# Kernel tuning notes

Hardware: AMD Instinct MI355X
Metric: run time of the kernel (lower is better)

The kernel has to match this reference:

```python
import math
import jax, jax.numpy as jnp
import numpy as np

DIM = 1024
B, T = 4, 2048


def setup_inputs() -> dict:
    key = jax.random.key(0)
    ks = jax.random.split(key, 7)
    std = 0.02
    x = jax.random.normal(ks[0], (B, T, DIM), dtype=jnp.float32)
    Wq = jax.random.normal(ks[1], (DIM, DIM), dtype=jnp.float32) * std
    Wk = jax.random.normal(ks[2], (DIM, DIM), dtype=jnp.float32) * std
    Wv = jax.random.normal(ks[3], (DIM, DIM), dtype=jnp.float32) * std
    Wo = jax.random.normal(ks[4], (DIM, DIM), dtype=jnp.float32) * std
    # decay_proj: torch init is zero weight, bias = decay_init; use a small random
    # weight so the data-dependent decay path is exercised.
    Wd = jax.random.normal(ks[5], (1, DIM), dtype=jnp.float32) * std
    bd = jnp.full((1,), 3.0, dtype=jnp.float32)  # decay_init
    out_scale = jnp.full((1,), 0.1, dtype=jnp.float32)
    return {"x": x, "Wq": Wq, "Wk": Wk, "Wv": Wv, "Wo": Wo,
            "Wd": Wd, "bd": bd, "out_scale": out_scale}


def reference(x, Wq, Wk, Wv, Wo, Wd, bd, out_scale):
    Bsz, Tlen, dim = x.shape
    scale = 1.0 / math.sqrt(dim)
    # torch Linear: y = x @ W.T
    q = jnp.einsum('btd,ed->bte', x, Wq)
    k = jnp.einsum('btd,ed->bte', x, Wk)
    v = jnp.einsum('btd,ed->bte', x, Wv)
    scores = jnp.einsum('btd,bsd->bts', q, k) * scale            # [B,T,T]
    decay_logits = jnp.einsum('btd,ed->bte', x, Wd)[..., 0] + bd  # [B,T]
    decay = jax.nn.sigmoid(decay_logits)
    pos = jnp.arange(Tlen)
    diff = pos[None, :] - pos[:, None]                            # diff[i,j] = j - i
    causal = (diff > 0).astype(x.dtype)                           # [T,T]
    log_decay = jnp.log(decay + 1e-8)                             # [B,T]
    dist = jnp.clip(diff.astype(x.dtype) - 1.0, 0.0)              # [T,T]
    # log_weights[b,i,j] = log_decay[b,j] * dist[i,j]
    log_weights = log_decay[:, None, :] * dist[None, :, :]
    weights = jnp.exp(log_weights) * causal[None, :, :]
    scores = scores * weights
    retrieved = jnp.einsum('bts,bsd->btd', scores, v)
    out = jnp.einsum('btd,ed->bte', retrieved, Wo) * out_scale
    return out
```

## Files before the change

### kernel.cpp

```cpp
#include <hip/hip_runtime.h>


using u16 = unsigned short;
typedef __bf16 bf16x8 __attribute__((ext_vector_type(8)));
typedef float f32x4 __attribute__((ext_vector_type(4)));

__device__ inline u16 f2bf(float f) {
  unsigned u = __builtin_bit_cast(unsigned, f);
  unsigned r = (u + 0x7FFFu + ((u >> 16) & 1u)) >> 16;
  return (u16)r;
}

__device__ inline void gload16(const u16* g, u16* l) {
  __builtin_amdgcn_global_load_lds(
      (const __attribute__((address_space(1))) void*)g,
      (__attribute__((address_space(3))) void*)l, 16, 0, 0);
}

__global__ __launch_bounds__(256) void xcast_decay(const float* __restrict__ x,
    u16* __restrict__ Xbf, const float* __restrict__ Wd,
    const float* __restrict__ bd, float* __restrict__ ldec) {
  int row = blockIdx.x;
  int t = threadIdx.x;
  float4 f = reinterpret_cast<const float4*>(x + (size_t)row * 1024)[t];
  float4 g = reinterpret_cast<const float4*>(Wd)[t];
  ushort4 o;
  o.x = f2bf(f.x); o.y = f2bf(f.y); o.z = f2bf(f.z); o.w = f2bf(f.w);
  reinterpret_cast<ushort4*>(Xbf + (size_t)row * 1024)[t] = o;
  float s = f.x * g.x + f.y * g.y + f.z * g.z + f.w * g.w;
  #pragma unroll
  for (int off = 32; off > 0; off >>= 1) s += __shfl_xor(s, off);
  __shared__ float red[4];
  if ((t & 63) == 0) red[t >> 6] = s;
  __syncthreads();
  if (t == 0) {
    float tot = red[0] + red[1] + red[2] + red[3];
    float dec = 1.f / (1.f + expf(-(tot + bd[0])));
    ldec[row] = logf(dec + 1e-8f);
  }
}

__global__ __launch_bounds__(256) void wcast(const float* __restrict__ Wq,
    const float* __restrict__ Wk, const float* __restrict__ Wv,
    const float* __restrict__ Wo, u16* __restrict__ Wall) {
  int b = blockIdx.x;
  int m = b >> 10;
  const float* src = (m == 0) ? Wq : (m == 1) ? Wk : (m == 2) ? Wv : Wo;
  int i = ((b & 1023) * 256 + threadIdx.x) * 4;
  float4 f = *reinterpret_cast<const float4*>(src + i);
  ushort4 o;
  o.x = f2bf(f.x); o.y = f2bf(f.y); o.z = f2bf(f.z); o.w = f2bf(f.w);
  *reinterpret_cast<ushort4*>(Wall + (size_t)m * 1048576 + i) = o;
}

template <int EPI>
__global__ __launch_bounds__(512, 2)
void gemm3(const u16* __restrict__ Ab, const u16* __restrict__ Bb,
           void* __restrict__ Cv, int lda, int ldb, int ldc, int K,
           int tiles_n, int diag, const float* __restrict__ ldec,
           const float* __restrict__ scale_ptr,
           long long abs_, long long bbs_, long long cbs_, int ld_stride) {
  __shared__ __align__(16) u16 lds2[73728];

  const int batch = blockIdx.y;
  const u16* A = Ab + (size_t)batch * abs_;
  const u16* B = Bb + (size_t)batch * bbs_;

  const int it = blockIdx.x / tiles_n;
  const int jt = blockIdx.x % tiles_n;
  if (EPI == 1 && jt < 2 * it) return;
  const int m0 = it * 256, n0 = jt * 128;

  const int tid = threadIdx.x;
  const int lane = tid & 63;
  const int w = tid >> 6;
  const int wm = w >> 1, wn = w & 1;
  const int l15 = lane & 15, lhi = lane >> 4;
  const int lr8 = lane >> 3;
  const int schunk = (lane & 7) ^ lr8;

  const int kt0 = diag ? it * 4 : 0;
  const int nkt = K / 64;
  const int span = nkt - kt0;

  f32x4 acc[4][4];
  #pragma unroll
  for (int i = 0; i < 4; ++i)
    #pragma unroll
    for (int j = 0; j < 4; ++j) acc[i][j] = (f32x4)0.f;

  auto stage = [&](int kt, int buf) {
    const size_t kb = (size_t)kt * 64 + schunk * 8;
    u16* lb = &lds2[buf * 24576];
    #pragma unroll
    for (int u = 0; u < 4; ++u)
      gload16(A + (size_t)(m0 + u * 64 + w * 8 + lr8) * lda + kb,
              lb + (u * 64 + w * 8) * 64);
    #pragma unroll
    for (int u = 0; u < 2; ++u)
      gload16(B + (size_t)(n0 + u * 64 + w * 8 + lr8) * ldb + kb,
              lb + 16384 + (u * 64 + w * 8) * 64);
  };

  stage(kt0, 0);
  stage(kt0 + 1, 1);
  asm volatile("s_waitcnt vmcnt(6)" ::: "memory");
  __builtin_amdgcn_s_barrier();

  int bR = 0, bS = 2;
  for (int t = 0; t < span; ++t) {
    const u16* baseA = &lds2[bR * 24576];
    const u16* baseB = baseA + 16384;

    bf16x8 af[4][2], bv[4][2];
    #pragma unroll
    for (int mi = 0; mi < 4; ++mi) {
      int r = wm * 64 + mi * 16 + l15;
      #pragma unroll
      for (int kk = 0; kk < 2; ++kk) {
        int s = (kk * 4 + lhi) ^ (r & 7);
        af[mi][kk] = *reinterpret_cast<const bf16x8*>(&baseA[r * 64 + s * 8]);
      }
    }
    #pragma unroll
    for (int ni = 0; ni < 4; ++ni) {
      int r = wn * 64 + ni * 16 + l15;
      #pragma unroll
      for (int kk = 0; kk < 2; ++kk) {
        int s = (kk * 4 + lhi) ^ (r & 7);
        bv[ni][kk] = *reinterpret_cast<const bf16x8*>(&baseB[r * 64 + s * 8]);
      }
    }

    int t2 = t + 2; if (t2 >= span) t2 = span - 1;
    stage(kt0 + t2, bS);

    __builtin_amdgcn_s_setprio(1);
    #pragma unroll
    for (int kk = 0; kk < 2; ++kk)
      #pragma unroll
      for (int mi = 0; mi < 4; ++mi)
        #pragma unroll
        for (int ni = 0; ni < 4; ++ni)
          acc[mi][ni] = __builtin_amdgcn_mfma_f32_16x16x32_bf16(
              af[mi][kk], bv[ni][kk], acc[mi][ni], 0, 0, 0);
    __builtin_amdgcn_s_setprio(0);

    asm volatile("s_waitcnt vmcnt(6)" ::: "memory");
    __builtin_amdgcn_s_barrier();

    bR = (bR == 2) ? 0 : bR + 1;
    bS = (bS == 2) ? 0 : bS + 1;
  }
  asm volatile("s_waitcnt vmcnt(0)" ::: "memory");

  if (EPI == 0) {
    u16* C = (u16*)Cv + (size_t)batch * cbs_;
    #pragma unroll
    for (int mi = 0; mi < 4; ++mi)
      #pragma unroll
      for (int q = 0; q < 4; ++q) {
        int row = m0 + wm * 64 + mi * 16 + lhi * 4 + q;
        u16* crow = C + (size_t)row * ldc + n0 + wn * 64 + l15;
        #pragma unroll
        for (int ni = 0; ni < 4; ++ni) crow[ni * 16] = f2bf(acc[mi][ni][q]);
      }
  } else if (EPI == 1) {
    u16* C = (u16*)Cv + (size_t)batch * cbs_;
    const float* ldp = ldec + (size_t)batch * ld_stride;
    float ldv[4];
    #pragma unroll
    for (int ni = 0; ni < 4; ++ni) ldv[ni] = ldp[n0 + wn * 64 + ni * 16 + l15];
    const float sc = 0.03125f;
    #pragma unroll
    for (int mi = 0; mi < 4; ++mi)
      #pragma unroll
      for (int q = 0; q < 4; ++q) {
        int row = m0 + wm * 64 + mi * 16 + lhi * 4 + q;
        u16* crow = C + (size_t)row * ldc + n0 + wn * 64 + l15;
        #pragma unroll
        for (int ni = 0; ni < 4; ++ni) {
          int col = n0 + wn * 64 + ni * 16 + l15;
          int d = col - row;
          float wgt = (d > 0) ? expf(ldv[ni] * (float)(d - 1)) : 0.f;
          crow[ni * 16] = f2bf(acc[mi][ni][q] * sc * wgt);
        }
      }
  } else {
    float* C = (float*)Cv + (size_t)batch * cbs_;
    const float sc = scale_ptr[0];
    #pragma unroll
    for (int mi = 0; mi < 4; ++mi)
      #pragma unroll
      for (int q = 0; q < 4; ++q) {
        int row = m0 + wm * 64 + mi * 16 + lhi * 4 + q;
        float* crow = C + (size_t)row * ldc + n0 + wn * 64 + l15;
        #pragma unroll
        for (int ni = 0; ni < 4; ++ni) crow[ni * 16] = acc[mi][ni][q] * sc;
      }
  }
}

extern "C" void kernel_launch(void* const* d_in, const int* in_sizes, int n_in,
                              void* d_out, int out_size, void* d_ws, size_t ws_size,
                              hipStream_t stream) {
  const float* x   = (const float*)d_in[0];
  const float* Wq  = (const float*)d_in[1];
  const float* Wk  = (const float*)d_in[2];
  const float* Wv  = (const float*)d_in[3];
  const float* Wo  = (const float*)d_in[4];
  const float* Wd  = (const float*)d_in[5];
  const float* bd  = (const float*)d_in[6];
  const float* osc = (const float*)d_in[7];
  float* out = (float*)d_out;

  char* ws = (char*)d_ws;
  size_t off = 0;
  u16* Xbf  = (u16*)(ws + off); off += (size_t)8192 * 1024 * 2;
  u16* Wall = (u16*)(ws + off); off += (size_t)4096 * 1024 * 2;
  u16* VT   = (u16*)(ws + off); off += (size_t)1024 * 8192 * 2;
  u16* S    = (u16*)(ws + off); off += (size_t)4 * 2048 * 2048 * 2;
  float* ldec = (float*)(ws + off); off += (size_t)8192 * 4;
  u16* QK   = (u16*)(ws + off); off += (size_t)8192 * 2048 * 2;
  u16* R    = QK;

  u16* Wqk = Wall;
  u16* Wvb = Wall + 2 * 1048576;
  u16* Wob = Wall + 3 * 1048576;

  xcast_decay<<<8192, 256, 0, stream>>>(x, Xbf, Wd, bd, ldec);
  wcast<<<4096, 256, 0, stream>>>(Wq, Wk, Wv, Wo, Wall);

  gemm3<0><<<dim3(32 * 16, 1), 512, 0, stream>>>(
      Xbf, Wqk, QK, 1024, 1024, 2048, 1024, 16, 0, nullptr, nullptr, 0, 0, 0, 0);

  gemm3<0><<<dim3(4 * 64, 1), 512, 0, stream>>>(
      Wvb, Xbf, VT, 1024, 1024, 8192, 1024, 64, 0, nullptr, nullptr, 0, 0, 0, 0);

  gemm3<1><<<dim3(8 * 16, 4), 512, 0, stream>>>(
      QK, QK + 1024, S, 2048, 2048, 2048, 1024, 16, 0, ldec, nullptr,
      4194304LL, 4194304LL, 4194304LL, 2048);

  gemm3<0><<<dim3(8 * 8, 4), 512, 0, stream>>>(
      S, VT, R, 2048, 8192, 1024, 2048, 8, 1, nullptr, nullptr,
      4194304LL, 2048LL, 2097152LL, 0);

  gemm3<2><<<dim3(32 * 8, 1), 512, 0, stream>>>(
      R, Wob, out, 1024, 1024, 1024, 1024, 8, 0, nullptr, osc, 0, 0, 0, 0);
}
```

Measured before the change: 177.3 us.

## Split GEMM into wide and 128x128 causal kernels with compact triangular grids

Splits the single GEMM template into two kernels. gemmW keeps 256x128 tiles for the projection GEMMs and interleaves half-tile loads with each k-substep. gemmN uses 128x128 tiles for the causal score and score×V GEMMs. The score GEMM now enumerates only upper-triangular tiles instead of launching and early-exiting lower ones, and the score×V GEMM reverses row order on half the batches to balance triangular work. This cuts wasted blocks and improves load balance, but drops the occupancy hint to one block per CU and adds extra barriers.

```diff
diff --git a/kernel.cpp b/kernel.cpp
--- a/kernel.cpp
+++ b/kernel.cpp
@@ -54,12 +54,11 @@
 }
 
 template <int EPI>
-__global__ __launch_bounds__(512, 2)
-void gemm3(const u16* __restrict__ Ab, const u16* __restrict__ Bb,
+__global__ __launch_bounds__(512, 1)
+void gemmW(const u16* __restrict__ Ab, const u16* __restrict__ Bb,
            void* __restrict__ Cv, int lda, int ldb, int ldc, int K,
-           int tiles_n, int diag, const float* __restrict__ ldec,
-           const float* __restrict__ scale_ptr,
-           long long abs_, long long bbs_, long long cbs_, int ld_stride) {
+           int tiles_n, const float* __restrict__ scale_ptr,
+           long long abs_, long long bbs_, long long cbs_) {
   __shared__ __align__(16) u16 lds2[73728];
 
   const int batch = blockIdx.y;
@@ -68,7 +67,6 @@
 
   const int it = blockIdx.x / tiles_n;
   const int jt = blockIdx.x % tiles_n;
-  if (EPI == 1 && jt < 2 * it) return;
   const int m0 = it * 256, n0 = jt * 128;
 
   const int tid = threadIdx.x;
@@ -79,9 +77,7 @@
   const int lr8 = lane >> 3;
   const int schunk = (lane & 7) ^ lr8;
 
-  const int kt0 = diag ? it * 4 : 0;
-  const int nkt = K / 64;
-  const int span = nkt - kt0;
+  const int span = K / 64;
 
   f32x4 acc[4][4];
   #pragma unroll
@@ -89,21 +85,22 @@
     #pragma unroll
     for (int j = 0; j < 4; ++j) acc[i][j] = (f32x4)0.f;
 
-  auto stage = [&](int kt, int buf) {
+  auto stageH = [&](int kt, int buf, int h) {
     const size_t kb = (size_t)kt * 64 + schunk * 8;
     u16* lb = &lds2[buf * 24576];
-    #pragma unroll
-    for (int u = 0; u < 4; ++u)
-      gload16(A + (size_t)(m0 + u * 64 + w * 8 + lr8) * lda + kb,
-              lb + (u * 64 + w * 8) * 64);
-    #pragma unroll
-    for (int u = 0; u < 2; ++u)
-      gload16(B + (size_t)(n0 + u * 64 + w * 8 + lr8) * ldb + kb,
-              lb + 16384 + (u * 64 + w * 8) * 64);
+    if (h == 0) {
+      gload16(A + (size_t)(m0 +       w * 8 + lr8) * lda + kb, lb + (w * 8) * 64);
+      gload16(A + (size_t)(m0 +  64 + w * 8 + lr8) * lda + kb, lb + (64 + w * 8) * 64);
+      gload16(B + (size_t)(n0 +       w * 8 + lr8) * ldb + kb, lb + 16384 + (w * 8) * 64);
+    } else {
+      gload16(A + (size_t)(m0 + 128 + w * 8 + lr8) * lda + kb, lb + (128 + w * 8) * 64);
+      gload16(A + (size_t)(m0 + 192 + w * 8 + lr8) * lda + kb, lb + (192 + w * 8) * 64);
+      gload16(B + (size_t)(n0 +  64 + w * 8 + lr8) * ldb + kb, lb + 16384 + (64 + w * 8) * 64);
+    }
   };
 
-  stage(kt0, 0);
-  stage(kt0 + 1, 1);
+  stageH(0, 0, 0); stageH(0, 0, 1);
+  stageH(1, 1, 0); stageH(1, 1, 1);
   asm volatile("s_waitcnt vmcnt(6)" ::: "memory");
   __builtin_amdgcn_s_barrier();
 
@@ -111,8 +108,131 @@
   for (int t = 0; t < span; ++t) {
     const u16* baseA = &lds2[bR * 24576];
     const u16* baseB = baseA + 16384;
-
-    bf16x8 af[4][2], bv[4][2];
+    int t2 = t + 2; if (t2 >= span) t2 = span - 1;
+
+    #pragma unroll
+    for (int kk = 0; kk < 2; ++kk) {
+      bf16x8 af[4], bv[4];
+      #pragma unroll
+      for (int mi = 0; mi < 4; ++mi) {
+        int r = wm * 64 + mi * 16 + l15;
+        int s = (kk * 4 + lhi) ^ (r & 7);
+        af[mi] = *reinterpret_cast<const bf16x8*>(&baseA[r * 64 + s * 8]);
+      }
+      #pragma unroll
+      for (int ni = 0; ni < 4; ++ni) {
+        int r = wn * 64 + ni * 16 + l15;
+        int s = (kk * 4 + lhi) ^ (r & 7);
+        bv[ni] = *reinterpret_cast<const bf16x8*>(&baseB[r * 64 + s * 8]);
+      }
+      stageH(t2, bS, kk);
+      __builtin_amdgcn_s_barrier();
+      __builtin_amdgcn_s_setprio(1);
+      #pragma unroll
+      for (int mi = 0; mi < 4; ++mi)
+        #pragma unroll
+        for (int ni = 0; ni < 4; ++ni)
+          acc[mi][ni] = __builtin_amdgcn_mfma_f32_16x16x32_bf16(
+              af[mi], bv[ni], acc[mi][ni], 0, 0, 0);
+      __builtin_amdgcn_s_setprio(0);
+      if (kk == 1) asm volatile("s_waitcnt vmcnt(6)" ::: "memory");
+      __builtin_amdgcn_s_barrier();
+    }
+
+    bR = (bR == 2) ? 0 : bR + 1;
+    bS = (bS == 2) ? 0 : bS + 1;
+  }
+  asm volatile("s_waitcnt vmcnt(0)" ::: "memory");
+
+  if (EPI == 0) {
+    u16* C = (u16*)Cv + (size_t)batch * cbs_;
+    #pragma unroll
+    for (int mi = 0; mi < 4; ++mi)
+      #pragma unroll
+      for (int q = 0; q < 4; ++q) {
+        int row = m0 + wm * 64 + mi * 16 + lhi * 4 + q;
+        u16* crow = C + (size_t)row * ldc + n0 + wn * 64 + l15;
+        #pragma unroll
+        for (int ni = 0; ni < 4; ++ni) crow[ni * 16] = f2bf(acc[mi][ni][q]);
+      }
+  } else {
+    float* C = (float*)Cv + (size_t)batch * cbs_;
+    const float sc = scale_ptr[0];
+    #pragma unroll
+    for (int mi = 0; mi < 4; ++mi)
+      #pragma unroll
+      for (int q = 0; q < 4; ++q) {
+        int row = m0 + wm * 64 + mi * 16 + lhi * 4 + q;
+        float* crow = C + (size_t)row * ldc + n0 + wn * 64 + l15;
+        #pragma unroll
+        for (int ni = 0; ni < 4; ++ni) crow[ni * 16] = acc[mi][ni][q] * sc;
+      }
+  }
+}
+
+template <int MODE>
+__global__ __launch_bounds__(512, 1)
+void gemmN(const u16* __restrict__ Ab, const u16* __restrict__ Bb,
+           void* __restrict__ Cv, int lda, int ldb, int ldc,
+           const float* __restrict__ ldec,
+           long long abs_, long long bbs_, long long cbs_) {
+  __shared__ __align__(16) u16 lds2[49152];
+
+  const int batch = blockIdx.y;
+  const u16* A = Ab + (size_t)batch * abs_;
+  const u16* B = Bb + (size_t)batch * bbs_;
+
+  int it, jt, kt0, span;
+  if (MODE == 1) {
+    int itr = blockIdx.x >> 3;
+    it = (batch >= 2) ? (15 - itr) : itr;
+    jt = blockIdx.x & 7;
+    kt0 = 2 * it;
+    span = 32 - 2 * it;
+  } else {
+    int L = blockIdx.x;
+    it = 0;
+    while (L >= 16 - it) { L -= 16 - it; ++it; }
+    jt = it + L;
+    kt0 = 0;
+    span = 16;
+  }
+  const int m0 = it * 128, n0 = jt * 128;
+
+  const int tid = threadIdx.x;
+  const int lane = tid & 63;
+  const int w = tid >> 6;
+  const int wm = w >> 2, wn = w & 3;
+  const int l15 = lane & 15, lhi = lane >> 4;
+  const int lr8 = lane >> 3;
+  const int schunk = (lane & 7) ^ lr8;
+
+  f32x4 acc[4][2];
+  #pragma unroll
+  for (int i = 0; i < 4; ++i)
+    #pragma unroll
+    for (int j = 0; j < 2; ++j) acc[i][j] = (f32x4)0.f;
+
+  auto stage = [&](int kt, int buf) {
+    const size_t kb = (size_t)kt * 64 + schunk * 8;
+    u16* lb = &lds2[buf * 16384];
+    gload16(A + (size_t)(m0 +      w * 8 + lr8) * lda + kb, lb + (w * 8) * 64);
+    gload16(A + (size_t)(m0 + 64 + w * 8 + lr8) * lda + kb, lb + (64 + w * 8) * 64);
+    gload16(B + (size_t)(n0 +      w * 8 + lr8) * ldb + kb, lb + 8192 + (w * 8) * 64);
+    gload16(B + (size_t)(n0 + 64 + w * 8 + lr8) * ldb + kb, lb + 8192 + (64 + w * 8) * 64);
+  };
+
+  stage(kt0, 0);
+  stage(kt0 + 1, 1);
+  asm volatile("s_waitcnt vmcnt(4)" ::: "memory");
+  __builtin_amdgcn_s_barrier();
+
+  int bR = 0, bS = 2;
+  for (int t = 0; t < span; ++t) {
+    const u16* baseA = &lds2[bR * 16384];
+    const u16* baseB = baseA + 8192;
+
+    bf16x8 af[4][2], bv[2][2];
     #pragma unroll
     for (int mi = 0; mi < 4; ++mi) {
       int r = wm * 64 + mi * 16 + l15;
@@ -123,8 +243,8 @@
       }
     }
     #pragma unroll
-    for (int ni = 0; ni < 4; ++ni) {
-      int r = wn * 64 + ni * 16 + l15;
+    for (int ni = 0; ni < 2; ++ni) {
+      int r = wn * 32 + ni * 16 + l15;
       #pragma unroll
       for (int kk = 0; kk < 2; ++kk) {
         int s = (kk * 4 + lhi) ^ (r & 7);
@@ -135,18 +255,18 @@
     int t2 = t + 2; if (t2 >= span) t2 = span - 1;
     stage(kt0 + t2, bS);
 
+    __builtin_amdgcn_s_barrier();
     __builtin_amdgcn_s_setprio(1);
     #pragma unroll
     for (int kk = 0; kk < 2; ++kk)
       #pragma unroll
       for (int mi = 0; mi < 4; ++mi)
         #pragma unroll
-        for (int ni = 0; ni < 4; ++ni)
+        for (int ni = 0; ni < 2; ++ni)
           acc[mi][ni] = __builtin_amdgcn_mfma_f32_16x16x32_bf16(
               af[mi][kk], bv[ni][kk], acc[mi][ni], 0, 0, 0);
     __builtin_amdgcn_s_setprio(0);
-
-    asm volatile("s_waitcnt vmcnt(6)" ::: "memory");
+    asm volatile("s_waitcnt vmcnt(4)" ::: "memory");
     __builtin_amdgcn_s_barrier();
 
     bR = (bR == 2) ? 0 : bR + 1;
@@ -154,49 +274,36 @@
   }
   asm volatile("s_waitcnt vmcnt(0)" ::: "memory");
 
-  if (EPI == 0) {
-    u16* C = (u16*)Cv + (size_t)batch * cbs_;
+  u16* C = (u16*)Cv + (size_t)batch * cbs_;
+  if (MODE == 1) {
     #pragma unroll
     for (int mi = 0; mi < 4; ++mi)
       #pragma unroll
       for (int q = 0; q < 4; ++q) {
         int row = m0 + wm * 64 + mi * 16 + lhi * 4 + q;
-        u16* crow = C + (size_t)row * ldc + n0 + wn * 64 + l15;
-        #pragma unroll
-        for (int ni = 0; ni < 4; ++ni) crow[ni * 16] = f2bf(acc[mi][ni][q]);
-      }
-  } else if (EPI == 1) {
-    u16* C = (u16*)Cv + (size_t)batch * cbs_;
-    const float* ldp = ldec + (size_t)batch * ld_stride;
-    float ldv[4];
-    #pragma unroll
-    for (int ni = 0; ni < 4; ++ni) ldv[ni] = ldp[n0 + wn * 64 + ni * 16 + l15];
+        u16* crow = C + (size_t)row * ldc + n0 + wn * 32 + l15;
+        #pragma unroll
+        for (int ni = 0; ni < 2; ++ni) crow[ni * 16] = f2bf(acc[mi][ni][q]);
+      }
+  } else {
+    const float* ldp = ldec + (size_t)batch * 2048;
+    float ldv[2];
+    #pragma unroll
+    for (int ni = 0; ni < 2; ++ni) ldv[ni] = ldp[n0 + wn * 32 + ni * 16 + l15];
     const float sc = 0.03125f;
     #pragma unroll
     for (int mi = 0; mi < 4; ++mi)
       #pragma unroll
       for (int q = 0; q < 4; ++q) {
         int row = m0 + wm * 64 + mi * 16 + lhi * 4 + q;
-        u16* crow = C + (size_t)row * ldc + n0 + wn * 64 + l15;
-        #pragma unroll
-        for (int ni = 0; ni < 4; ++ni) {
-          int col = n0 + wn * 64 + ni * 16 + l15;
+        u16* crow = C + (size_t)row * ldc + n0 + wn * 32 + l15;
+        #pragma unroll
+        for (int ni = 0; ni < 2; ++ni) {
+          int col = n0 + wn * 32 + ni * 16 + l15;
           int d = col - row;
           float wgt = (d > 0) ? expf(ldv[ni] * (float)(d - 1)) : 0.f;
           crow[ni * 16] = f2bf(acc[mi][ni][q] * sc * wgt);
         }
-      }
-  } else {
-    float* C = (float*)Cv + (size_t)batch * cbs_;
-    const float sc = scale_ptr[0];
-    #pragma unroll
-    for (int mi = 0; mi < 4; ++mi)
-      #pragma unroll
-      for (int q = 0; q < 4; ++q) {
-        int row = m0 + wm * 64 + mi * 16 + lhi * 4 + q;
-        float* crow = C + (size_t)row * ldc + n0 + wn * 64 + l15;
-        #pragma unroll
-        for (int ni = 0; ni < 4; ++ni) crow[ni * 16] = acc[mi][ni][q] * sc;
       }
   }
 }
@@ -231,20 +338,20 @@
   xcast_decay<<<8192, 256, 0, stream>>>(x, Xbf, Wd, bd, ldec);
   wcast<<<4096, 256, 0, stream>>>(Wq, Wk, Wv, Wo, Wall);
 
-  gemm3<0><<<dim3(32 * 16, 1), 512, 0, stream>>>(
-      Xbf, Wqk, QK, 1024, 1024, 2048, 1024, 16, 0, nullptr, nullptr, 0, 0, 0, 0);
-
-  gemm3<0><<<dim3(4 * 64, 1), 512, 0, stream>>>(
-      Wvb, Xbf, VT, 1024, 1024, 8192, 1024, 64, 0, nullptr, nullptr, 0, 0, 0, 0);
-
-  gemm3<1><<<dim3(8 * 16, 4), 512, 0, stream>>>(
-      QK, QK + 1024, S, 2048, 2048, 2048, 1024, 16, 0, ldec, nullptr,
-      4194304LL, 4194304LL, 4194304LL, 2048);
-
-  gemm3<0><<<dim3(8 * 8, 4), 512, 0, stream>>>(
-      S, VT, R, 2048, 8192, 1024, 2048, 8, 1, nullptr, nullptr,
-      4194304LL, 2048LL, 2097152LL, 0);
-
-  gemm3<2><<<dim3(32 * 8, 1), 512, 0, stream>>>(
-      R, Wob, out, 1024, 1024, 1024, 1024, 8, 0, nullptr, osc, 0, 0, 0, 0);
-}
+  gemmW<0><<<dim3(512, 1), 512, 0, stream>>>(
+      Xbf, Wqk, QK, 1024, 1024, 2048, 1024, 16, nullptr, 0, 0, 0);
+
+  gemmW<0><<<dim3(256, 1), 512, 0, stream>>>(
+      Wvb, Xbf, VT, 1024, 1024, 8192, 1024, 64, nullptr, 0, 0, 0);
+
+  gemmN<2><<<dim3(136, 4), 512, 0, stream>>>(
+      QK, QK + 1024, S, 2048, 2048, 2048, ldec,
+      4194304LL, 4194304LL, 4194304LL);
+
+  gemmN<1><<<dim3(128, 4), 512, 0, stream>>>(
+      S, VT, R, 2048, 8192, 1024, nullptr,
+      4194304LL, 2048LL, 2097152LL);
+
+  gemmW<2><<<dim3(256, 1), 512, 0, stream>>>(
+      R, Wob, out, 1024, 1024, 1024, 1024, 8, osc, 0, 0, 0);
+}
```

Measured after the change: 186.5 us. 5.2% more time.

## Use 256x256 tiles with XCD swizzle, triangular scheduling, and split-K for S·V

Applied to the files above, without the earlier changes.

Every GEMM moves from 256x128 tiles to 256x256 tiles, with 8 waves each computing 128x64. The pipeline goes from triple to double buffering, and one block runs per CU. Block indices are remapped so neighbouring tiles land on the same XCD, and the causal score GEMM launches only the upper-triangular tiles instead of exiting early. The diagonal-heavy S·V GEMM splits K for its first row blocks into fp32 partials, and a new add kernel sums them, to balance the uneven causal work. The cost is more register pressure, lower occupancy, and an extra launch plus fp32 traffic.

```diff
diff --git a/kernel.cpp b/kernel.cpp
--- a/kernel.cpp
+++ b/kernel.cpp
@@ -15,6 +15,12 @@
   __builtin_amdgcn_global_load_lds(
       (const __attribute__((address_space(1))) void*)g,
       (__attribute__((address_space(3))) void*)l, 16, 0, 0);
+}
+
+__device__ __forceinline__ int xcd_swz(int o, int n) {
+  int q = n >> 3, r = n & 7;
+  int xcd = o & 7, slot = o >> 3;
+  return (xcd < r ? xcd * (q + 1) : r * (q + 1) + (xcd - r) * q) + slot;
 }
 
 __global__ __launch_bounds__(256) void xcast_decay(const float* __restrict__ x,
@@ -53,75 +59,90 @@
   *reinterpret_cast<ushort4*>(Wall + (size_t)m * 1048576 + i) = o;
 }
 
-template <int EPI>
-__global__ __launch_bounds__(512, 2)
-void gemm3(const u16* __restrict__ Ab, const u16* __restrict__ Bb,
+__global__ __launch_bounds__(256) void radd(const float* __restrict__ p0,
+    const float* __restrict__ p1, u16* __restrict__ R) {
+  size_t i = ((size_t)blockIdx.x * 256 + threadIdx.x) * 4;
+  float4 a = *reinterpret_cast<const float4*>(p0 + i);
+  float4 b = *reinterpret_cast<const float4*>(p1 + i);
+  size_t batch = i >> 20, within = i & 1048575;
+  ushort4 o;
+  o.x = f2bf(a.x + b.x); o.y = f2bf(a.y + b.y);
+  o.z = f2bf(a.z + b.z); o.w = f2bf(a.w + b.w);
+  *reinterpret_cast<ushort4*>(R + batch * 2097152 + within) = o;
+}
+
+template <int MODE>
+__global__ __launch_bounds__(512, 1)
+void gemmX(const u16* __restrict__ Ab, const u16* __restrict__ Bb,
            void* __restrict__ Cv, int lda, int ldb, int ldc, int K,
-           int tiles_n, int diag, const float* __restrict__ ldec,
+           int tiles_n, const float* __restrict__ ldec,
            const float* __restrict__ scale_ptr,
-           long long abs_, long long bbs_, long long cbs_, int ld_stride) {
-  __shared__ __align__(16) u16 lds2[73728];
+           float* __restrict__ aux0, float* __restrict__ aux1,
+           long long abs_, long long bbs_, long long cbs_) {
+  __shared__ __align__(16) u16 lds2[65536];
 
   const int batch = blockIdx.y;
   const u16* A = Ab + (size_t)batch * abs_;
   const u16* B = Bb + (size_t)batch * bbs_;
 
-  const int it = blockIdx.x / tiles_n;
-  const int jt = blockIdx.x % tiles_n;
-  if (EPI == 1 && jt < 2 * it) return;
-  const int m0 = it * 256, n0 = jt * 128;
+  const int bx = xcd_swz(blockIdx.x, gridDim.x);
+  int it, jt, kt0, kend, ks = 0; bool part = false;
+  if (MODE == 0 || MODE == 3) {
+    it = bx / tiles_n; jt = bx % tiles_n; kt0 = 0; kend = K / 64;
+  } else if (MODE == 1) {
+    int L = bx; it = 0;
+    while (L >= 8 - it) { L -= 8 - it; ++it; }
+    jt = it + L; kt0 = 0; kend = 16;
+  } else {
+    if (bx < 32) {
+      it = bx >> 3; jt = (bx >> 1) & 3; ks = bx & 1; part = true;
+      kt0 = ks ? 16 : it * 4; kend = ks ? 32 : 16;
+    } else {
+      int z = bx - 32; it = 4 + (z >> 2); jt = z & 3;
+      kt0 = it * 4; kend = 32;
+    }
+  }
+  const int m0 = it * 256, n0 = jt * 256;
 
   const int tid = threadIdx.x;
   const int lane = tid & 63;
   const int w = tid >> 6;
-  const int wm = w >> 1, wn = w & 1;
+  const int wm = w >> 2, wn = w & 3;
   const int l15 = lane & 15, lhi = lane >> 4;
-  const int lr8 = lane >> 3;
-  const int schunk = (lane & 7) ^ lr8;
-
-  const int kt0 = diag ? it * 4 : 0;
-  const int nkt = K / 64;
-  const int span = nkt - kt0;
-
-  f32x4 acc[4][4];
+  const int l8 = lane >> 3;
+  const int gch = (lane & 7) ^ (l8 & 7);
+
+  f32x4 acc[8][4];
   #pragma unroll
-  for (int i = 0; i < 4; ++i)
+  for (int i = 0; i < 8; ++i)
     #pragma unroll
     for (int j = 0; j < 4; ++j) acc[i][j] = (f32x4)0.f;
 
   auto stage = [&](int kt, int buf) {
-    const size_t kb = (size_t)kt * 64 + schunk * 8;
-    u16* lb = &lds2[buf * 24576];
+    const size_t kb = (size_t)kt * 64 + gch * 8;
+    u16* la = &lds2[buf * 16384];
+    u16* lb = &lds2[32768 + buf * 16384];
     #pragma unroll
     for (int u = 0; u < 4; ++u)
-      gload16(A + (size_t)(m0 + u * 64 + w * 8 + lr8) * lda + kb,
-              lb + (u * 64 + w * 8) * 64);
-    #pragma unroll
-    for (int u = 0; u < 2; ++u)
-      gload16(B + (size_t)(n0 + u * 64 + w * 8 + lr8) * ldb + kb,
-              lb + 16384 + (u * 64 + w * 8) * 64);
+      gload16(A + (size_t)(m0 + u * 64 + w * 8 + l8) * lda + kb, la + u * 4096 + w * 512);
+    #pragma unroll
+    for (int u = 0; u < 4; ++u)
+      gload16(B + (size_t)(n0 + u * 64 + w * 8 + l8) * ldb + kb, lb + u * 4096 + w * 512);
   };
 
   stage(kt0, 0);
-  stage(kt0 + 1, 1);
-  asm volatile("s_waitcnt vmcnt(6)" ::: "memory");
+  asm volatile("s_waitcnt vmcnt(0)" ::: "memory");
   __builtin_amdgcn_s_barrier();
 
-  int bR = 0, bS = 2;
+  const int span = kend - kt0;
   for (int t = 0; t < span; ++t) {
-    const u16* baseA = &lds2[bR * 24576];
-    const u16* baseB = baseA + 16384;
-
-    bf16x8 af[4][2], bv[4][2];
-    #pragma unroll
-    for (int mi = 0; mi < 4; ++mi) {
-      int r = wm * 64 + mi * 16 + l15;
-      #pragma unroll
-      for (int kk = 0; kk < 2; ++kk) {
-        int s = (kk * 4 + lhi) ^ (r & 7);
-        af[mi][kk] = *reinterpret_cast<const bf16x8*>(&baseA[r * 64 + s * 8]);
-      }
-    }
+    const int buf = t & 1;
+    if (t + 1 < span) stage(kt0 + t + 1, buf ^ 1);
+
+    const u16* baseA = &lds2[buf * 16384];
+    const u16* baseB = &lds2[32768 + buf * 16384];
+
+    bf16x8 bv[4][2];
     #pragma unroll
     for (int ni = 0; ni < 4; ++ni) {
       int r = wn * 64 + ni * 16 + l15;
@@ -131,52 +152,48 @@
         bv[ni][kk] = *reinterpret_cast<const bf16x8*>(&baseB[r * 64 + s * 8]);
       }
     }
-
-    int t2 = t + 2; if (t2 >= span) t2 = span - 1;
-    stage(kt0 + t2, bS);
-
     __builtin_amdgcn_s_setprio(1);
     #pragma unroll
-    for (int kk = 0; kk < 2; ++kk)
-      #pragma unroll
-      for (int mi = 0; mi < 4; ++mi)
-        #pragma unroll
-        for (int ni = 0; ni < 4; ++ni)
-          acc[mi][ni] = __builtin_amdgcn_mfma_f32_16x16x32_bf16(
-              af[mi][kk], bv[ni][kk], acc[mi][ni], 0, 0, 0);
+    for (int mi = 0; mi < 8; ++mi) {
+      int r = wm * 128 + mi * 16 + l15;
+      int s0 = lhi ^ (r & 7), s1 = (4 + lhi) ^ (r & 7);
+      bf16x8 a0 = *reinterpret_cast<const bf16x8*>(&baseA[r * 64 + s0 * 8]);
+      bf16x8 a1 = *reinterpret_cast<const bf16x8*>(&baseA[r * 64 + s1 * 8]);
+      #pragma unroll
+      for (int ni = 0; ni < 4; ++ni)
+        acc[mi][ni] = __builtin_amdgcn_mfma_f32_16x16x32_bf16(a0, bv[ni][0], acc[mi][ni], 0, 0, 0);
+      #pragma unroll
+      for (int ni = 0; ni < 4; ++ni)
+        acc[mi][ni] = __builtin_amdgcn_mfma_f32_16x16x32_bf16(a1, bv[ni][1], acc[mi][ni], 0, 0, 0);
+    }
     __builtin_amdgcn_s_setprio(0);
-
-    asm volatile("s_waitcnt vmcnt(6)" ::: "memory");
+    asm volatile("s_waitcnt vmcnt(0)" ::: "memory");
     __builtin_amdgcn_s_barrier();
-
-    bR = (bR == 2) ? 0 : bR + 1;
-    bS = (bS == 2) ? 0 : bS + 1;
-  }
-  asm volatile("s_waitcnt vmcnt(0)" ::: "memory");
-
-  if (EPI == 0) {
+  }
+
+  if (MODE == 0) {
     u16* C = (u16*)Cv + (size_t)batch * cbs_;
     #pragma unroll
-    for (int mi = 0; mi < 4; ++mi)
+    for (int mi = 0; mi < 8; ++mi)
       #pragma unroll
       for (int q = 0; q < 4; ++q) {
-        int row = m0 + wm * 64 + mi * 16 + lhi * 4 + q;
+        int row = m0 + wm * 128 + mi * 16 + lhi * 4 + q;
         u16* crow = C + (size_t)row * ldc + n0 + wn * 64 + l15;
         #pragma unroll
         for (int ni = 0; ni < 4; ++ni) crow[ni * 16] = f2bf(acc[mi][ni][q]);
       }
-  } else if (EPI == 1) {
+  } else if (MODE == 1) {
     u16* C = (u16*)Cv + (size_t)batch * cbs_;
-    const float* ldp = ldec + (size_t)batch * ld_stride;
+    const float* ldp = ldec + (size_t)batch * 2048;
     float ldv[4];
     #pragma unroll
     for (int ni = 0; ni < 4; ++ni) ldv[ni] = ldp[n0 + wn * 64 + ni * 16 + l15];
     const float sc = 0.03125f;
     #pragma unroll
-    for (int mi = 0; mi < 4; ++mi)
+    for (int mi = 0; mi < 8; ++mi)
       #pragma unroll
       for (int q = 0; q < 4; ++q) {
-        int row = m0 + wm * 64 + mi * 16 + lhi * 4 + q;
+        int row = m0 + wm * 128 + mi * 16 + lhi * 4 + q;
         u16* crow = C + (size_t)row * ldc + n0 + wn * 64 + l15;
         #pragma unroll
         for (int ni = 0; ni < 4; ++ni) {
@@ -186,14 +203,38 @@
           crow[ni * 16] = f2bf(acc[mi][ni][q] * sc * wgt);
         }
       }
+  } else if (MODE == 2) {
+    if (part) {
+      float* P = (ks ? aux1 : aux0) + (size_t)batch * 1048576;
+      #pragma unroll
+      for (int mi = 0; mi < 8; ++mi)
+        #pragma unroll
+        for (int q = 0; q < 4; ++q) {
+          int row = m0 + wm * 128 + mi * 16 + lhi * 4 + q;
+          float* crow = P + (size_t)row * 1024 + n0 + wn * 64 + l15;
+          #pragma unroll
+          for (int ni = 0; ni < 4; ++ni) crow[ni * 16] = acc[mi][ni][q];
+        }
+    } else {
+      u16* C = (u16*)Cv + (size_t)batch * cbs_;
+      #pragma unroll
+      for (int mi = 0; mi < 8; ++mi)
+        #pragma unroll
+        for (int q = 0; q < 4; ++q) {
+          int row = m0 + wm * 128 + mi * 16 + lhi * 4 + q;
+          u16* crow = C + (size_t)row * ldc + n0 + wn * 64 + l15;
+          #pragma unroll
+          for (int ni = 0; ni < 4; ++ni) crow[ni * 16] = f2bf(acc[mi][ni][q]);
+        }
+    }
   } else {
     float* C = (float*)Cv + (size_t)batch * cbs_;
     const float sc = scale_ptr[0];
     #pragma unroll
-    for (int mi = 0; mi < 4; ++mi)
+    for (int mi = 0; mi < 8; ++mi)
       #pragma unroll
       for (int q = 0; q < 4; ++q) {
-        int row = m0 + wm * 64 + mi * 16 + lhi * 4 + q;
+        int row = m0 + wm * 128 + mi * 16 + lhi * 4 + q;
         float* crow = C + (size_t)row * ldc + n0 + wn * 64 + l15;
         #pragma unroll
         for (int ni = 0; ni < 4; ++ni) crow[ni * 16] = acc[mi][ni][q] * sc;
@@ -223,6 +264,8 @@
   float* ldec = (float*)(ws + off); off += (size_t)8192 * 4;
   u16* QK   = (u16*)(ws + off); off += (size_t)8192 * 2048 * 2;
   u16* R    = QK;
+  float* Rp0 = (float*)Xbf;
+  float* Rp1 = (float*)((char*)QK + 16777216);
 
   u16* Wqk = Wall;
   u16* Wvb = Wall + 2 * 1048576;
@@ -231,20 +274,25 @@
   xcast_decay<<<8192, 256, 0, stream>>>(x, Xbf, Wd, bd, ldec);
   wcast<<<4096, 256, 0, stream>>>(Wq, Wk, Wv, Wo, Wall);
 
-  gemm3<0><<<dim3(32 * 16, 1), 512, 0, stream>>>(
-      Xbf, Wqk, QK, 1024, 1024, 2048, 1024, 16, 0, nullptr, nullptr, 0, 0, 0, 0);
-
-  gemm3<0><<<dim3(4 * 64, 1), 512, 0, stream>>>(
-      Wvb, Xbf, VT, 1024, 1024, 8192, 1024, 64, 0, nullptr, nullptr, 0, 0, 0, 0);
-
-  gemm3<1><<<dim3(8 * 16, 4), 512, 0, stream>>>(
-      QK, QK + 1024, S, 2048, 2048, 2048, 1024, 16, 0, ldec, nullptr,
-      4194304LL, 4194304LL, 4194304LL, 2048);
-
-  gemm3<0><<<dim3(8 * 8, 4), 512, 0, stream>>>(
-      S, VT, R, 2048, 8192, 1024, 2048, 8, 1, nullptr, nullptr,
-      4194304LL, 2048LL, 2097152LL, 0);
-
-  gemm3<2><<<dim3(32 * 8, 1), 512, 0, stream>>>(
-      R, Wob, out, 1024, 1024, 1024, 1024, 8, 0, nullptr, osc, 0, 0, 0, 0);
-}
+  gemmX<0><<<dim3(256, 1), 512, 0, stream>>>(
+      Xbf, Wqk, QK, 1024, 1024, 2048, 1024, 8, nullptr, nullptr, nullptr, nullptr,
+      0, 0, 0);
+
+  gemmX<0><<<dim3(128, 1), 512, 0, stream>>>(
+      Wvb, Xbf, VT, 1024, 1024, 8192, 1024, 32, nullptr, nullptr, nullptr, nullptr,
+      0, 0, 0);
+
+  gemmX<1><<<dim3(36, 4), 512, 0, stream>>>(
+      QK, QK + 1024, S, 2048, 2048, 2048, 1024, 0, ldec, nullptr, nullptr, nullptr,
+      4194304LL, 4194304LL, 4194304LL);
+
+  gemmX<2><<<dim3(48, 4), 512, 0, stream>>>(
+      S, VT, R, 2048, 8192, 1024, 2048, 0, nullptr, nullptr, Rp0, Rp1,
+      4194304LL, 2048LL, 2097152LL);
+
+  radd<<<4096, 256, 0, stream>>>(Rp0, Rp1, R);
+
+  gemmX<3><<<dim3(128, 1), 512, 0, stream>>>(
+      R, Wob, out, 1024, 1024, 1024, 1024, 4, nullptr, osc, nullptr, nullptr,
+      0, 0, 0);
+}
```

After: 207.0 us. 1.17x slower.

## Shrink GEMM tiles to 128x128 with double buffering and merge cast kernels

Applied to the files above, without the earlier changes.

Replaces the 256x128 tile, 512-thread, triple-buffered GEMM with a 128x128 tile, 256-thread, double-buffered version that uses less LDS. The goal is more concurrent blocks per CU and finer causal skipping in the score and retrieval GEMMs. It also reverses the row order for half the batches in the triangular S·V GEMM to balance load, and merges the two cast kernels into one launch. In exchange, each block reuses less data, the pipeline is shallower, and it waits for all loads (vmcnt(0)) every iteration.

```diff
diff --git a/kernel.cpp b/kernel.cpp
--- a/kernel.cpp
+++ b/kernel.cpp
@@ -17,69 +17,71 @@
       (__attribute__((address_space(3))) void*)l, 16, 0, 0);
 }
 
-__global__ __launch_bounds__(256) void xcast_decay(const float* __restrict__ x,
+__global__ __launch_bounds__(256) void prep(const float* __restrict__ x,
     u16* __restrict__ Xbf, const float* __restrict__ Wd,
-    const float* __restrict__ bd, float* __restrict__ ldec) {
-  int row = blockIdx.x;
+    const float* __restrict__ bd, float* __restrict__ ldec,
+    const float* __restrict__ Wq, const float* __restrict__ Wk,
+    const float* __restrict__ Wv, const float* __restrict__ Wo,
+    u16* __restrict__ Wall) {
+  int b = blockIdx.x;
   int t = threadIdx.x;
-  float4 f = reinterpret_cast<const float4*>(x + (size_t)row * 1024)[t];
-  float4 g = reinterpret_cast<const float4*>(Wd)[t];
-  ushort4 o;
-  o.x = f2bf(f.x); o.y = f2bf(f.y); o.z = f2bf(f.z); o.w = f2bf(f.w);
-  reinterpret_cast<ushort4*>(Xbf + (size_t)row * 1024)[t] = o;
-  float s = f.x * g.x + f.y * g.y + f.z * g.z + f.w * g.w;
-  #pragma unroll
-  for (int off = 32; off > 0; off >>= 1) s += __shfl_xor(s, off);
-  __shared__ float red[4];
-  if ((t & 63) == 0) red[t >> 6] = s;
-  __syncthreads();
-  if (t == 0) {
-    float tot = red[0] + red[1] + red[2] + red[3];
-    float dec = 1.f / (1.f + expf(-(tot + bd[0])));
-    ldec[row] = logf(dec + 1e-8f);
+  if (b < 8192) {
+    float4 f = reinterpret_cast<const float4*>(x + (size_t)b * 1024)[t];
+    float4 g = reinterpret_cast<const float4*>(Wd)[t];
+    ushort4 o;
+    o.x = f2bf(f.x); o.y = f2bf(f.y); o.z = f2bf(f.z); o.w = f2bf(f.w);
+    reinterpret_cast<ushort4*>(Xbf + (size_t)b * 1024)[t] = o;
+    float s = f.x * g.x + f.y * g.y + f.z * g.z + f.w * g.w;
+    #pragma unroll
+    for (int off = 32; off > 0; off >>= 1) s += __shfl_xor(s, off);
+    __shared__ float red[4];
+    if ((t & 63) == 0) red[t >> 6] = s;
+    __syncthreads();
+    if (t == 0) {
+      float tot = red[0] + red[1] + red[2] + red[3];
+      float dec = 1.f / (1.f + expf(-(tot + bd[0])));
+      ldec[b] = logf(dec + 1e-8f);
+    }
+  } else {
+    int wb = b - 8192;
+    int m = wb >> 10;
+    const float* src = (m == 0) ? Wq : (m == 1) ? Wk : (m == 2) ? Wv : Wo;
+    int i = ((wb & 1023) * 256 + t) * 4;
+    float4 f = *reinterpret_cast<const float4*>(src + i);
+    ushort4 o;
+    o.x = f2bf(f.x); o.y = f2bf(f.y); o.z = f2bf(f.z); o.w = f2bf(f.w);
+    *reinterpret_cast<ushort4*>(Wall + (size_t)m * 1048576 + i) = o;
   }
 }
 
-__global__ __launch_bounds__(256) void wcast(const float* __restrict__ Wq,
-    const float* __restrict__ Wk, const float* __restrict__ Wv,
-    const float* __restrict__ Wo, u16* __restrict__ Wall) {
-  int b = blockIdx.x;
-  int m = b >> 10;
-  const float* src = (m == 0) ? Wq : (m == 1) ? Wk : (m == 2) ? Wv : Wo;
-  int i = ((b & 1023) * 256 + threadIdx.x) * 4;
-  float4 f = *reinterpret_cast<const float4*>(src + i);
-  ushort4 o;
-  o.x = f2bf(f.x); o.y = f2bf(f.y); o.z = f2bf(f.z); o.w = f2bf(f.w);
-  *reinterpret_cast<ushort4*>(Wall + (size_t)m * 1048576 + i) = o;
-}
-
 template <int EPI>
-__global__ __launch_bounds__(512, 2)
-void gemm3(const u16* __restrict__ Ab, const u16* __restrict__ Bb,
+__global__ __launch_bounds__(256, 2)
+void gemmP(const u16* __restrict__ Ab, const u16* __restrict__ Bb,
            void* __restrict__ Cv, int lda, int ldb, int ldc, int K,
-           int tiles_n, int diag, const float* __restrict__ ldec,
+           int tiles_n, int diag, int flip, const float* __restrict__ ldec,
            const float* __restrict__ scale_ptr,
-           long long abs_, long long bbs_, long long cbs_, int ld_stride) {
-  __shared__ __align__(16) u16 lds2[73728];
+           long long abs_, long long bbs_, long long cbs_) {
+  __shared__ __align__(16) u16 lds2[32768];
 
   const int batch = blockIdx.y;
   const u16* A = Ab + (size_t)batch * abs_;
   const u16* B = Bb + (size_t)batch * bbs_;
 
-  const int it = blockIdx.x / tiles_n;
+  int it = blockIdx.x / tiles_n;
   const int jt = blockIdx.x % tiles_n;
-  if (EPI == 1 && jt < 2 * it) return;
-  const int m0 = it * 256, n0 = jt * 128;
+  if (flip && batch >= 2) it = (gridDim.x / tiles_n - 1) - it;
+  if (EPI == 1 && jt < it) return;
+  const int m0 = it * 128, n0 = jt * 128;
 
   const int tid = threadIdx.x;
   const int lane = tid & 63;
   const int w = tid >> 6;
-  const int wm = w >> 1, wn = w & 1;
+  const int wm = (w >> 1) * 64, wn = (w & 1) * 64;
   const int l15 = lane & 15, lhi = lane >> 4;
   const int lr8 = lane >> 3;
   const int schunk = (lane & 7) ^ lr8;
 
-  const int kt0 = diag ? it * 4 : 0;
+  const int kt0 = diag ? it * 2 : 0;
   const int nkt = K / 64;
   const int span = nkt - kt0;
 
@@ -91,31 +93,32 @@
 
   auto stage = [&](int kt, int buf) {
     const size_t kb = (size_t)kt * 64 + schunk * 8;
-    u16* lb = &lds2[buf * 24576];
+    u16* la = &lds2[buf * 16384];
+    u16* lb = la + 8192;
     #pragma unroll
     for (int u = 0; u < 4; ++u)
-      gload16(A + (size_t)(m0 + u * 64 + w * 8 + lr8) * lda + kb,
-              lb + (u * 64 + w * 8) * 64);
-    #pragma unroll
-    for (int u = 0; u < 2; ++u)
-      gload16(B + (size_t)(n0 + u * 64 + w * 8 + lr8) * ldb + kb,
-              lb + 16384 + (u * 64 + w * 8) * 64);
+      gload16(A + (size_t)(m0 + u * 32 + w * 8 + lr8) * lda + kb,
+              la + (u * 32 + w * 8) * 64);
+    #pragma unroll
+    for (int u = 0; u < 4; ++u)
+      gload16(B + (size_t)(n0 + u * 32 + w * 8 + lr8) * ldb + kb,
+              lb + (u * 32 + w * 8) * 64);
   };
 
   stage(kt0, 0);
-  stage(kt0 + 1, 1);
-  asm volatile("s_waitcnt vmcnt(6)" ::: "memory");
+  asm volatile("s_waitcnt vmcnt(0)" ::: "memory");
   __builtin_amdgcn_s_barrier();
 
-  int bR = 0, bS = 2;
   for (int t = 0; t < span; ++t) {
-    const u16* baseA = &lds2[bR * 24576];
-    const u16* baseB = baseA + 16384;
-
+    const int buf = t & 1;
+    if (t + 1 < span) stage(kt0 + t + 1, buf ^ 1);
+
+    const u16* baseA = &lds2[buf * 16384];
+    const u16* baseB = baseA + 8192;
     bf16x8 af[4][2], bv[4][2];
     #pragma unroll
     for (int mi = 0; mi < 4; ++mi) {
-      int r = wm * 64 + mi * 16 + l15;
+      int r = wm + mi * 16 + l15;
       #pragma unroll
       for (int kk = 0; kk < 2; ++kk) {
         int s = (kk * 4 + lhi) ^ (r & 7);
@@ -124,16 +127,13 @@
     }
     #pragma unroll
     for (int ni = 0; ni < 4; ++ni) {
-      int r = wn * 64 + ni * 16 + l15;
+      int r = wn + ni * 16 + l15;
       #pragma unroll
       for (int kk = 0; kk < 2; ++kk) {
         int s = (kk * 4 + lhi) ^ (r & 7);
         bv[ni][kk] = *reinterpret_cast<const bf16x8*>(&baseB[r * 64 + s * 8]);
       }
     }
-
-    int t2 = t + 2; if (t2 >= span) t2 = span - 1;
-    stage(kt0 + t2, bS);
 
     __builtin_amdgcn_s_setprio(1);
     #pragma unroll
@@ -146,13 +146,9 @@
               af[mi][kk], bv[ni][kk], acc[mi][ni], 0, 0, 0);
     __builtin_amdgcn_s_setprio(0);
 
-    asm volatile("s_waitcnt vmcnt(6)" ::: "memory");
+    asm volatile("s_waitcnt vmcnt(0)" ::: "memory");
     __builtin_amdgcn_s_barrier();
-
-    bR = (bR == 2) ? 0 : bR + 1;
-    bS = (bS == 2) ? 0 : bS + 1;
   }
-  asm volatile("s_waitcnt vmcnt(0)" ::: "memory");
 
   if (EPI == 0) {
     u16* C = (u16*)Cv + (size_t)batch * cbs_;
@@ -160,27 +156,27 @@
     for (int mi = 0; mi < 4; ++mi)
       #pragma unroll
       for (int q = 0; q < 4; ++q) {
-        int row = m0 + wm * 64 + mi * 16 + lhi * 4 + q;
-        u16* crow = C + (size_t)row * ldc + n0 + wn * 64 + l15;
+        int row = m0 + wm + mi * 16 + lhi * 4 + q;
+        u16* crow = C + (size_t)row * ldc + n0 + wn + l15;
         #pragma unroll
         for (int ni = 0; ni < 4; ++ni) crow[ni * 16] = f2bf(acc[mi][ni][q]);
       }
   } else if (EPI == 1) {
     u16* C = (u16*)Cv + (size_t)batch * cbs_;
-    const float* ldp = ldec + (size_t)batch * ld_stride;
+    const float* ldp = ldec + (size_t)batch * 2048;
     float ldv[4];
     #pragma unroll
-    for (int ni = 0; ni < 4; ++ni) ldv[ni] = ldp[n0 + wn * 64 + ni * 16 + l15];
+    for (int ni = 0; ni < 4; ++ni) ldv[ni] = ldp[n0 + wn + ni * 16 + l15];
     const float sc = 0.03125f;
     #pragma unroll
     for (int mi = 0; mi < 4; ++mi)
       #pragma unroll
       for (int q = 0; q < 4; ++q) {
-        int row = m0 + wm * 64 + mi * 16 + lhi * 4 + q;
-        u16* crow = C + (size_t)row * ldc + n0 + wn * 64 + l15;
+        int row = m0 + wm + mi * 16 + lhi * 4 + q;
+        u16* crow = C + (size_t)row * ldc + n0 + wn + l15;
         #pragma unroll
         for (int ni = 0; ni < 4; ++ni) {
-          int col = n0 + wn * 64 + ni * 16 + l15;
+          int col = n0 + wn + ni * 16 + l15;
           int d = col - row;
           float wgt = (d > 0) ? expf(ldv[ni] * (float)(d - 1)) : 0.f;
           crow[ni * 16] = f2bf(acc[mi][ni][q] * sc * wgt);
@@ -193,8 +189,8 @@
     for (int mi = 0; mi < 4; ++mi)
       #pragma unroll
       for (int q = 0; q < 4; ++q) {
-        int row = m0 + wm * 64 + mi * 16 + lhi * 4 + q;
-        float* crow = C + (size_t)row * ldc + n0 + wn * 64 + l15;
+        int row = m0 + wm + mi * 16 + lhi * 4 + q;
+        float* crow = C + (size_t)row * ldc + n0 + wn + l15;
         #pragma unroll
         for (int ni = 0; ni < 4; ++ni) crow[ni * 16] = acc[mi][ni][q] * sc;
       }
@@ -228,23 +224,25 @@
   u16* Wvb = Wall + 2 * 1048576;
   u16* Wob = Wall + 3 * 1048576;
 
-  xcast_decay<<<8192, 256, 0, stream>>>(x, Xbf, Wd, bd, ldec);
-  wcast<<<4096, 256, 0, stream>>>(Wq, Wk, Wv, Wo, Wall);
-
-  gemm3<0><<<dim3(32 * 16, 1), 512, 0, stream>>>(
-      Xbf, Wqk, QK, 1024, 1024, 2048, 1024, 16, 0, nullptr, nullptr, 0, 0, 0, 0);
-
-  gemm3<0><<<dim3(4 * 64, 1), 512, 0, stream>>>(
-      Wvb, Xbf, VT, 1024, 1024, 8192, 1024, 64, 0, nullptr, nullptr, 0, 0, 0, 0);
-
-  gemm3<1><<<dim3(8 * 16, 4), 512, 0, stream>>>(
-      QK, QK + 1024, S, 2048, 2048, 2048, 1024, 16, 0, ldec, nullptr,
-      4194304LL, 4194304LL, 4194304LL, 2048);
-
-  gemm3<0><<<dim3(8 * 8, 4), 512, 0, stream>>>(
-      S, VT, R, 2048, 8192, 1024, 2048, 8, 1, nullptr, nullptr,
-      4194304LL, 2048LL, 2097152LL, 0);
-
-  gemm3<2><<<dim3(32 * 8, 1), 512, 0, stream>>>(
-      R, Wob, out, 1024, 1024, 1024, 1024, 8, 0, nullptr, osc, 0, 0, 0, 0);
-}
+  prep<<<12288, 256, 0, stream>>>(x, Xbf, Wd, bd, ldec, Wq, Wk, Wv, Wo, Wall);
+
+  gemmP<0><<<dim3(64 * 16, 1), 256, 0, stream>>>(
+      Xbf, Wqk, QK, 1024, 1024, 2048, 1024, 16, 0, 0, nullptr, nullptr,
+      0, 0, 0);
+
+  gemmP<0><<<dim3(8 * 64, 1), 256, 0, stream>>>(
+      Wvb, Xbf, VT, 1024, 1024, 8192, 1024, 64, 0, 0, nullptr, nullptr,
+      0, 0, 0);
+
+  gemmP<1><<<dim3(16 * 16, 4), 256, 0, stream>>>(
+      QK, QK + 1024, S, 2048, 2048, 2048, 1024, 16, 0, 0, ldec, nullptr,
+      4194304LL, 4194304LL, 4194304LL);
+
+  gemmP<0><<<dim3(16 * 8, 4), 256, 0, stream>>>(
+      S, VT, R, 2048, 8192, 1024, 2048, 8, 1, 1, nullptr, nullptr,
+      4194304LL, 2048LL, 2097152LL);
+
+  gemmP<2><<<dim3(64 * 8, 1), 256, 0, stream>>>(
+      R, Wob, out, 1024, 1024, 1024, 1024, 8, 0, 0, nullptr, osc,
+      0, 0, 0);
+}
```

Result: faster. 164.8 us (median of 2 runs) (-7.1%).
